# Optimization experiments

Measured on AMD Instinct MI355X. Metric: run time of the kernel, lower is better.

## Reference

```python
import jax, jax.numpy as jnp
import numpy as np

L, CIN, CKV, E, H, D, NQ, NK = 3, 128, 256, 128, 8, 16, 4096, 1024
CLAMP_MAX = 65503.0  # torch.clamp(max=65503)
SCALE = 1.0 / (D * D)  # non-standard: 1 / projection_dim**2


def group_norm(x, w, b, groups, eps=1e-5):
    # x: [..., C, N]; w, b broadcastable to x.shape[:-1] (i.e. lead + (C,))
    lead = x.shape[:-2]
    C, N = x.shape[-2:]
    xg = x.reshape(lead + (groups, C // groups, N))
    mu = xg.mean(axis=(-2, -1), keepdims=True)
    var = ((xg - mu) ** 2).mean(axis=(-2, -1), keepdims=True)
    xn = ((xg - mu) * jax.lax.rsqrt(var + eps)).reshape(lead + (C, N))
    return xn * w[..., None] + b[..., None]


def split_heads(t):
    # [L, 1, E, N] -> [L, 1, H, N, D]
    l, b, e, n = t.shape
    return t.transpose(0, 1, 3, 2).reshape(l, b, n, H, D).transpose(0, 1, 3, 2, 4)


def setup_inputs():
    key = jax.random.key(0)
    ks = jax.random.split(key, 18)
    r = lambda k, s: jax.random.normal(k, s, dtype=jnp.float32)
    return {
        'x': r(ks[0], (1, CIN, NQ)),
        'x_global': r(ks[1], (L, CKV, NK)),
        'xyz': r(ks[2], (1, NQ, 3)),
        'xyz_global': r(ks[3], (L, NK, 3)),
        'gn1_w': r(ks[4], (CIN,)), 'gn1_b': r(ks[5], (CIN,)),
        'gn2_w': r(ks[6], (L, CKV)), 'gn2_b': r(ks[7], (L, CKV)),
        'qw': r(ks[8], (L, E, CIN)) * 0.05, 'qb': r(ks[9], (L, E)),
        'kw': r(ks[10], (L, E, CKV)) * 0.05, 'kb': r(ks[11], (L, E)),
        'vw': r(ks[12], (L, E, CKV)) * 0.05, 'vb': r(ks[13], (L, E)),
        'qgn_w': r(ks[14], (L, E)), 'qgn_b': r(ks[15], (L, E)),
        'cw': r(ks[16], (L, CIN, E)) * 0.05, 'cb': r(ks[17], (L, CIN)),
    }


def reference(x, x_global, xyz, xyz_global, gn1_w, gn1_b, gn2_w, gn2_b,
              qw, qb, kw, kb, vw, vb, qgn_w, qgn_b, cw, cb):
    # pre-norm of query features (shared across layers): [1, CIN, NQ]
    xq = jax.nn.relu(group_norm(x, gn1_w, gn1_b, 8))
    # per-source KV features: [L, 1, CKV, NK]
    xg = jax.nn.relu(group_norm(x_global[:, None], gn2_w[:, None], gn2_b[:, None], 16))

    # conv1d (kernel=1) projections + the shared q_gn GroupNorm(8, E)
    q = jnp.einsum('lec,bcn->lben', qw, xq) + qb[:, None, :, None]        # [L,1,E,NQ]
    q = group_norm(q, qgn_w[:, None], qgn_b[:, None], 8)
    k = jnp.einsum('lec,lbcn->lben', kw, xg) + kb[:, None, :, None]       # [L,1,E,NK]
    k = group_norm(k, qgn_w[:, None], qgn_b[:, None], 8)
    v = jnp.einsum('lec,lbcn->lben', vw, xg) + vb[:, None, :, None]       # [L,1,E,NK]
    v = group_norm(v, qgn_w[:, None], qgn_b[:, None], 8)

    qh, kh, vh = split_heads(q), split_heads(k), split_heads(v)           # [L,1,H,*,D]

    score = jnp.einsum('lbhqd,lbhkd->lbhqk', qh * SCALE, kh)              # [L,1,H,NQ,NK]
    score = jnp.minimum(score, CLAMP_MAX)
    w_att = jax.nn.softmax(score, axis=-1)
    o = jnp.einsum('lbhqk,lbhkd->lbhqd', w_att, vh)                        # [L,1,H,NQ,D]
    o = o.transpose(0, 1, 3, 2, 4).reshape(L, 1, NQ, E)                    # merge heads
    o = jnp.einsum('lbqe,loe->lbqo', o, cw) + cb[:, None, None, :]         # combine heads
    o = o.transpose(0, 1, 3, 2) + xq[None]                                 # [L,1,CIN,NQ], SA residual

    out = o.mean(axis=0) + x                                               # mean over sources + block residual
    return out, w_att[-1]                                                  # weight of last layer, as in torch loop
```

## Files before the change

### kernel.cpp

```cpp
#include <hip/hip_runtime.h>
#include <math.h>

constexpr int NQ = 4096, NK = 1024, CIN = 128, CKV = 256, E = 128, H = 8, D = 16, LAYERS = 3;
constexpr float SCALE = 1.0f / 256.0f;
constexpr float CLAMP_MAX = 65503.0f;
constexpr float LOG2E = 1.44269504088896340736f;
constexpr float CLAMP2 = CLAMP_MAX * LOG2E;

typedef __bf16 bf16x8 __attribute__((ext_vector_type(8)));
typedef __bf16 bf16x4 __attribute__((ext_vector_type(4)));
typedef float f32x16 __attribute__((ext_vector_type(16)));
typedef float f32x4 __attribute__((ext_vector_type(4)));

__device__ __forceinline__ float exp2_fast(float x) {
#if __has_builtin(__builtin_amdgcn_exp2f)
  return __builtin_amdgcn_exp2f(x);
#else
  return exp2f(x);
#endif
}

__device__ __forceinline__ void block_reduce2(float& a, float& b, float* red) {
#pragma unroll
  for (int off = 32; off > 0; off >>= 1) {
    a += __shfl_down(a, off, 64);
    b += __shfl_down(b, off, 64);
  }
  int lane = threadIdx.x & 63, wid = threadIdx.x >> 6;
  if (lane == 0) { red[wid * 2] = a; red[wid * 2 + 1] = b; }
  __syncthreads();
  if (threadIdx.x == 0) {
    float sa = 0.f, sb = 0.f;
#pragma unroll
    for (int w = 0; w < 4; w++) { sa += red[w * 2]; sb += red[w * 2 + 1]; }
    red[0] = sa; red[1] = sb;
  }
  __syncthreads();
  a = red[0]; b = red[1];
}

__global__ __launch_bounds__(256) void pre_partial(const float* __restrict__ x,
                                                   const float* __restrict__ xg,
                                                   float* __restrict__ acc) {
  __shared__ float red[8];
  int b = blockIdx.x, t = threadIdx.x;
  const float4* p;
  int aidx;
  if (b < 256) { p = (const float4*)x + (size_t)b * 512; aidx = b >> 5; }
  else { int i = b - 256; p = (const float4*)xg + (size_t)i * 512; aidx = 8 + (i >> 3); }
  float s = 0.f, sq = 0.f;
#pragma unroll
  for (int i = 0; i < 2; i++) {
    float4 v = p[t + i * 256];
    s += v.x + v.y + v.z + v.w;
    sq += v.x * v.x + v.y * v.y + v.z * v.z + v.w * v.w;
  }
  block_reduce2(s, sq, red);
  if (t == 0) {
    atomicAdd(&acc[aidx * 2], s);
    atomicAdd(&acc[aidx * 2 + 1], sq);
  }
}

__global__ __launch_bounds__(256) void stage_a(const float* __restrict__ x,
                                               const float* __restrict__ xg,
                                               const float* __restrict__ acc,
                                               const float* __restrict__ gn1w,
                                               const float* __restrict__ gn1b,
                                               const float* __restrict__ gn2w,
                                               const float* __restrict__ gn2b,
                                               const float* __restrict__ qw,
                                               const float* __restrict__ kw,
                                               const float* __restrict__ vw,
                                               __bf16* __restrict__ xq_t,
                                               __bf16* __restrict__ xg_t,
                                               __bf16* __restrict__ qwb,
                                               __bf16* __restrict__ kwb,
                                               __bf16* __restrict__ vwb) {
  int b = blockIdx.x, t = threadIdx.x;
  if (b >= 320) {
    int i = b - 320;
    const float* src; __bf16* dst; int off;
    if (i < 24)      { src = qw; dst = qwb; off = i * 2048; }
    else if (i < 72) { src = kw; dst = kwb; off = (i - 24) * 2048; }
    else             { src = vw; dst = vwb; off = (i - 72) * 2048; }
    int base = off + t * 8;
    float4 a = *(const float4*)(src + base);
    float4 c = *(const float4*)(src + base + 4);
    bf16x8 o = { (__bf16)a.x, (__bf16)a.y, (__bf16)a.z, (__bf16)a.w,
                 (__bf16)c.x, (__bf16)c.y, (__bf16)c.z, (__bf16)c.w };
    *(bf16x8*)(dst + base) = o;
    return;
  }
  __shared__ float T[128 * 36];
  const float* in; __bf16* out; int N, Cout, ccbase, n0, gbase;
  const float* gw; const float* gb; float inv;
  if (b < 128) {
    in = x; N = NQ; out = xq_t; Cout = 128; ccbase = 0; n0 = b * 32;
    gw = gn1w; gb = gn1b; gbase = 0; inv = 1.f / 65536.f;
  } else {
    int i = b - 128; int l = i / 64; int r = i % 64; int ch = r >> 5;
    n0 = (r & 31) * 32;
    in = xg + ((size_t)l * 256 + ch * 128) * 1024; N = NK;
    out = xg_t + (size_t)l * 1024 * 256; Cout = 256; ccbase = ch * 128;
    gw = gn2w + l * 256 + ch * 128; gb = gn2b + l * 256 + ch * 128;
    gbase = 8 + l * 16 + ch * 8; inv = 1.f / 16384.f;
  }
  int nq = t & 7, cbase = t >> 3;
#pragma unroll
  for (int i = 0; i < 4; i++) {
    int c = cbase + 32 * i;
    int g = gbase + (c >> 4);
    float mu = acc[2 * g] * inv;
    float rs = rsqrtf(acc[2 * g + 1] * inv - mu * mu + 1e-5f);
    float sc = gw[c] * rs, sh = gb[c] - mu * sc;
    float4 v = *(const float4*)(in + (size_t)c * N + n0 + nq * 4);
    float4 o;
    o.x = fmaxf(v.x * sc + sh, 0.f);
    o.y = fmaxf(v.y * sc + sh, 0.f);
    o.z = fmaxf(v.z * sc + sh, 0.f);
    o.w = fmaxf(v.w * sc + sh, 0.f);
    *(float4*)(T + c * 36 + nq * 4) = o;
  }
  __syncthreads();
  int n = t >> 3, c0 = (t & 7) * 16;
  bf16x8 o1, o2;
#pragma unroll
  for (int j = 0; j < 8; j++) {
    o1[j] = (__bf16)T[(c0 + j) * 36 + n];
    o2[j] = (__bf16)T[(c0 + 8 + j) * 36 + n];
  }
  __bf16* op = out + (size_t)(n0 + n) * Cout + ccbase + c0;
  *(bf16x8*)op = o1;
  *(bf16x8*)(op + 8) = o2;
}

template <int KSTEPS>
__device__ __forceinline__ void gemm_tile(const __bf16* __restrict__ A,
                                          const __bf16* __restrict__ Bm,
                                          int stride, f32x16& acc, int l31, int half) {
#pragma unroll
  for (int ks = 0; ks < KSTEPS; ks++) {
    bf16x8 af = *(const bf16x8*)(A + (size_t)l31 * stride + ks * 16 + half * 8);
    bf16x8 bf = *(const bf16x8*)(Bm + (size_t)l31 * stride + ks * 16 + half * 8);
    acc = __builtin_amdgcn_mfma_f32_32x32x16_bf16(af, bf, acc, 0, 0, 0);
  }
}

__global__ __launch_bounds__(256) void proj_mfma(const __bf16* __restrict__ xq_t,
                                                 const __bf16* __restrict__ xg_t,
                                                 const __bf16* __restrict__ qwb,
                                                 const __bf16* __restrict__ kwb,
                                                 const __bf16* __restrict__ vwb,
                                                 const float* __restrict__ qb,
                                                 const float* __restrict__ kb,
                                                 const float* __restrict__ vb,
                                                 __bf16* __restrict__ q_raw,
                                                 __bf16* __restrict__ k_raw,
                                                 __bf16* __restrict__ v_raw,
                                                 float* __restrict__ qgnAcc) {
  int t = threadIdx.x;
  int w = blockIdx.x * 4 + (t >> 6);
  int lane = t & 63, l31 = lane & 31, half = lane >> 5;
  f32x16 acc = {0.f,0.f,0.f,0.f,0.f,0.f,0.f,0.f,0.f,0.f,0.f,0.f,0.f,0.f,0.f,0.f};
  int mat, l, e0, n0, N;
  const __bf16* A; const __bf16* Bm; const float* bias;
  if (w < 1536) {
    mat = 0; l = w >> 9; int r = w & 511; e0 = (r & 3) * 32; n0 = (r >> 2) * 32;
    N = NQ; A = qwb + (size_t)l * 128 * 128; Bm = xq_t; bias = qb + l * 128;
  } else if (w < 1920) {
    mat = 1; int idx = w - 1536; l = idx >> 7; int r = idx & 127;
    e0 = (r & 3) * 32; n0 = (r >> 2) * 32;
    N = NK; A = kwb + (size_t)l * 128 * 256; Bm = xg_t + (size_t)l * 1024 * 256;
    bias = kb + l * 128;
  } else {
    mat = 2; int idx = w - 1920; l = idx >> 7; int r = idx & 127;
    e0 = (r & 3) * 32; n0 = (r >> 2) * 32;
    N = NK; A = vwb + (size_t)l * 128 * 256; Bm = xg_t + (size_t)l * 1024 * 256;
    bias = vb + l * 128;
  }
  if (mat == 0) {
    gemm_tile<8>(A + (size_t)e0 * 128, Bm + (size_t)n0 * 128, 128, acc, l31, half);
  } else {
    gemm_tile<16>(A + (size_t)e0 * 256, Bm + (size_t)n0 * 256, 256, acc, l31, half);
  }

  float vals[16];
  float s0 = 0.f, sq0 = 0.f, s1 = 0.f, sq1 = 0.f;
#pragma unroll
  for (int r = 0; r < 16; r++) {
    int row = (r & 3) + 8 * (r >> 2) + 4 * half;
    float v = acc[r] + bias[e0 + row];
    vals[r] = v;
    if (r < 8) { s0 += v; sq0 += v * v; } else { s1 += v; sq1 += v * v; }
  }
#pragma unroll
  for (int off = 1; off < 64; off <<= 1) {
    s0 += __shfl_xor(s0, off); sq0 += __shfl_xor(sq0, off);
    s1 += __shfl_xor(s1, off); sq1 += __shfl_xor(sq1, off);
  }
  int gbase = (mat == 0 ? 0 : (mat == 1 ? 24 : 48)) + l * 8 + (e0 >> 4);
  if (lane == 0) {
    atomicAdd(&qgnAcc[gbase * 2], s0);
    atomicAdd(&qgnAcc[gbase * 2 + 1], sq0);
    atomicAdd(&qgnAcc[(gbase + 1) * 2], s1);
    atomicAdd(&qgnAcc[(gbase + 1) * 2 + 1], sq1);
  }
  if (mat < 2) {
    __bf16* out = (mat == 0 ? q_raw : k_raw);
#pragma unroll
    for (int qd = 0; qd < 4; qd++) {
      int h = (e0 >> 4) + (qd >> 1);
      int d0 = 4 * half + 8 * (qd & 1);
      bf16x4 o;
#pragma unroll
      for (int j = 0; j < 4; j++) o[j] = (__bf16)vals[qd * 4 + j];
      *(bf16x4*)(out + ((size_t)(l * 8 + h) * N + n0 + l31) * 16 + d0) = o;
    }
  } else {
#pragma unroll
    for (int r = 0; r < 16; r++) {
      int row = (r & 3) + 8 * (r >> 2) + 4 * half;
      int h = (e0 >> 4) + (row >> 4);
      v_raw[((size_t)(l * 8 + h) * 16 + (row & 15)) * NK + n0 + l31] = (__bf16)vals[r];
    }
  }
}

__global__ __launch_bounds__(256) void attn_kernel(const __bf16* __restrict__ qbf,
                                                   const __bf16* __restrict__ kbf,
                                                   const __bf16* __restrict__ vbf,
                                                   const float* __restrict__ qgnAcc,
                                                   const float* __restrict__ qgnw,
                                                   const float* __restrict__ qgnb,
                                                   float* __restrict__ ob,
                                                   float* __restrict__ rinv_ws) {
  __shared__ __bf16 Pt[4][32 * 40];
  __shared__ float rinv_s[4][32];

  const int t = threadIdx.x;
  const int wv = t >> 6;
  const int lane = t & 63;
  const int l31 = lane & 31, half = lane >> 5, l15 = lane & 15, quad = lane >> 4;
  const int h = blockIdx.y, l = blockIdx.z;
  const int q0 = blockIdx.x * 128 + wv * 32;

  const __bf16* Qh = qbf + (size_t)(l * H + h) * NQ * D;
  const __bf16* Kh = kbf + (size_t)(l * H + h) * NK * D;
  const __bf16* Vh = vbf + (size_t)(l * H + h) * D * NK;

  const int gq = l * 8 + h, gk = 24 + l * 8 + h, gv = 48 + l * 8 + h;
  const float invq = 1.f / 65536.f, invkv = 1.f / 16384.f;
  const float muq = qgnAcc[2 * gq] * invq;
  const float rsq = rsqrtf(qgnAcc[2 * gq + 1] * invq - muq * muq + 1e-5f);
  const float muk = qgnAcc[2 * gk] * invkv;
  const float rsk = rsqrtf(qgnAcc[2 * gk + 1] * invkv - muk * muk + 1e-5f);
  const float muv = qgnAcc[2 * gv] * invkv;
  const float rsv = rsqrtf(qgnAcc[2 * gv + 1] * invkv - muv * muv + 1e-5f);

  const int cbase = l * 128 + h * 16;
  float ka[8], kc[8];
  bf16x8 qfrag;
  {
    const float EX = SCALE * LOG2E;
    bf16x8 qraw = *(const bf16x8*)(Qh + (size_t)(q0 + l31) * D + half * 8);
#pragma unroll
    for (int j = 0; j < 8; j++) {
      float w = qgnw[cbase + half * 8 + j], bb = qgnb[cbase + half * 8 + j];
      float wq = w * rsq;
      qfrag[j] = (__bf16)((float)qraw[j] * (wq * EX) + (bb - muq * wq) * EX);
      float wk = w * rsk;
      ka[j] = wk; kc[j] = bb - muk * wk;
    }
  }
  const float va = qgnw[cbase + l15] * rsv;
  const float vc = qgnb[cbase + l15] - muv * va;

  f32x4 oa0 = {0.f, 0.f, 0.f, 0.f}, oa1 = {0.f, 0.f, 0.f, 0.f};
  float rsum[16];
#pragma unroll
  for (int r = 0; r < 16; ++r) rsum[r] = 0.f;

  __bf16* Pw = &Pt[wv][0];

  for (int c = 0; c < 32; ++c) {
    const int k0 = c * 32;
    bf16x8 kraw = *(const bf16x8*)(Kh + (size_t)(k0 + l31) * D + half * 8);
    bf16x8 kf;
#pragma unroll
    for (int j = 0; j < 8; j++) kf[j] = (__bf16)((float)kraw[j] * ka[j] + kc[j]);
    f32x16 s = {0.f,0.f,0.f,0.f,0.f,0.f,0.f,0.f,0.f,0.f,0.f,0.f,0.f,0.f,0.f,0.f};
    s = __builtin_amdgcn_mfma_f32_32x32x16_bf16(qfrag, kf, s, 0, 0, 0);
#pragma unroll
    for (int r = 0; r < 16; ++r) {
      float p = exp2_fast(fminf(s[r], CLAMP2));
      rsum[r] += p;
      int row = (r & 3) + 8 * (r >> 2) + 4 * half;
      Pw[row * 40 + l31] = (__bf16)p;
    }
    bf16x8 vraw = *(const bf16x8*)(Vh + (size_t)l15 * NK + k0 + quad * 8);
    bf16x8 bv;
#pragma unroll
    for (int j = 0; j < 8; j++) bv[j] = (__bf16)((float)vraw[j] * va + vc);
    bf16x8 a0 = *(const bf16x8*)(Pw + l15 * 40 + quad * 8);
    bf16x8 a1 = *(const bf16x8*)(Pw + (16 + l15) * 40 + quad * 8);
    oa0 = __builtin_amdgcn_mfma_f32_16x16x32_bf16(a0, bv, oa0, 0, 0, 0);
    oa1 = __builtin_amdgcn_mfma_f32_16x16x32_bf16(a1, bv, oa1, 0, 0, 0);
  }

#pragma unroll
  for (int r = 0; r < 16; ++r) {
    float v = rsum[r];
    v += __shfl_xor(v, 1); v += __shfl_xor(v, 2); v += __shfl_xor(v, 4);
    v += __shfl_xor(v, 8); v += __shfl_xor(v, 16);
    rsum[r] = v;
  }
  if (l31 == 0) {
#pragma unroll
    for (int r = 0; r < 16; ++r)
      rinv_s[wv][(r & 3) + 8 * (r >> 2) + 4 * half] = 1.f / rsum[r];
  }

  float* Ow = (float*)Pw;
#pragma unroll
  for (int r = 0; r < 4; ++r) {
    int qa = quad * 4 + r;
    Ow[l15 * 36 + qa] = oa0[r] * rinv_s[wv][qa];
    Ow[l15 * 36 + 16 + qa] = oa1[r] * rinv_s[wv][16 + qa];
  }
  if (l == 2 && lane < 32)
    rinv_ws[(size_t)h * NQ + q0 + lane] = rinv_s[wv][lane];
  {
    int dd = lane >> 2, j = (lane & 3) * 8;
    float4 u0 = *(const float4*)(Ow + dd * 36 + j);
    float4 u1 = *(const float4*)(Ow + dd * 36 + j + 4);
    size_t rb = (size_t)(l * E + h * D + dd) * NQ + q0 + j;
    *(float4*)(ob + rb) = u0;
    *(float4*)(ob + rb + 4) = u1;
  }
}

__global__ __launch_bounds__(256) void post_kernel(const __bf16* __restrict__ qbf,
                                                   const __bf16* __restrict__ kbf,
                                                   const float* __restrict__ rinv_ws,
                                                   const float* __restrict__ qgnAcc,
                                                   const float* __restrict__ qgnw,
                                                   const float* __restrict__ qgnb,
                                                   const float* __restrict__ x,
                                                   const float* __restrict__ accAll,
                                                   const float* __restrict__ gn1w,
                                                   const float* __restrict__ gn1b,
                                                   const float* __restrict__ ob,
                                                   const float* __restrict__ cw,
                                                   const float* __restrict__ cb,
                                                   float* __restrict__ out,
                                                   float* __restrict__ wout) {
  __shared__ float S[128 * 16];
  const int blk = blockIdx.x, t = threadIdx.x;
  if (blk < 512) {
    const int wv = t >> 6, lane = t & 63;
    const int l31 = lane & 31, half = lane >> 5;
    const int qtile = blk & 31, h = (blk >> 5) & 7, khalf = blk >> 8;
    const int q0 = qtile * 128 + wv * 32;
    const int kbase = khalf * 512;

    const __bf16* Qh = qbf + (size_t)(2 * H + h) * NQ * D;
    const __bf16* Kh = kbf + (size_t)(2 * H + h) * NK * D;

    const int gq = 16 + h, gk = 24 + 16 + h;
    const float invq = 1.f / 65536.f, invkv = 1.f / 16384.f;
    const float muq = qgnAcc[2 * gq] * invq;
    const float rsq = rsqrtf(qgnAcc[2 * gq + 1] * invq - muq * muq + 1e-5f);
    const float muk = qgnAcc[2 * gk] * invkv;
    const float rsk = rsqrtf(qgnAcc[2 * gk + 1] * invkv - muk * muk + 1e-5f);

    const int cbase = 2 * 128 + h * 16;
    float ka[8], kc[8];
    bf16x8 qfrag;
    {
      const float EX = SCALE * LOG2E;
      bf16x8 qraw = *(const bf16x8*)(Qh + (size_t)(q0 + l31) * D + half * 8);
#pragma unroll
      for (int j = 0; j < 8; j++) {
        float w = qgnw[cbase + half * 8 + j], bb = qgnb[cbase + half * 8 + j];
        float wq = w * rsq;
        qfrag[j] = (__bf16)((float)qraw[j] * (wq * EX) + (bb - muq * wq) * EX);
        float wk = w * rsk;
        ka[j] = wk; kc[j] = bb - muk * wk;
      }
    }

    float riv[16];
#pragma unroll
    for (int r = 0; r < 16; ++r)
      riv[r] = rinv_ws[(size_t)h * NQ + q0 + (r & 3) + 8 * (r >> 2) + 4 * half];

    for (int c = 0; c < 16; ++c) {
      const int k0 = kbase + c * 32;
      bf16x8 kraw = *(const bf16x8*)(Kh + (size_t)(k0 + l31) * D + half * 8);
      bf16x8 kf;
#pragma unroll
      for (int j = 0; j < 8; j++) kf[j] = (__bf16)((float)kraw[j] * ka[j] + kc[j]);
      f32x16 s = {0.f,0.f,0.f,0.f,0.f,0.f,0.f,0.f,0.f,0.f,0.f,0.f,0.f,0.f,0.f,0.f};
      s = __builtin_amdgcn_mfma_f32_32x32x16_bf16(qfrag, kf, s, 0, 0, 0);
#pragma unroll
      for (int r = 0; r < 16; ++r) {
        float p = exp2_fast(fminf(s[r], CLAMP2)) * riv[r];
        int row = (r & 3) + 8 * (r >> 2) + 4 * half;
        __builtin_nontemporal_store(p, &wout[(size_t)(h * NQ + q0 + row) * NK + k0 + l31]);
      }
    }
    return;
  }

  const int nt0 = (blk - 512) * 16;
  const int c0 = (t >> 2) * 2;
  const int nf = t & 3;
  float4 a0 = make_float4(0.f, 0.f, 0.f, 0.f);
  float4 a1 = make_float4(0.f, 0.f, 0.f, 0.f);
  for (int l = 0; l < LAYERS; l++) {
    if (l) __syncthreads();
#pragma unroll
    for (int i = 0; i < 2; i++) {
      int fid = i * 256 + t;
      int e = fid >> 2, pos = fid & 3;
      *(float4*)(S + e * 16 + pos * 4) =
          *(const float4*)(ob + ((size_t)l * E + e) * NQ + nt0 + pos * 4);
    }
    __syncthreads();
    const float* cwl = cw + (size_t)l * CIN * E;
#pragma unroll 8
    for (int e4 = 0; e4 < E / 4; e4++) {
      const int e = e4 * 4;
      float4 w0 = *(const float4*)(cwl + (size_t)c0 * E + e);
      float4 w1 = *(const float4*)(cwl + (size_t)(c0 + 1) * E + e);
      float4 s0 = *(const float4*)(S + (e + 0) * 16 + nf * 4);
      float4 s1 = *(const float4*)(S + (e + 1) * 16 + nf * 4);
      float4 s2 = *(const float4*)(S + (e + 2) * 16 + nf * 4);
      float4 s3 = *(const float4*)(S + (e + 3) * 16 + nf * 4);
      a0.x += w0.x * s0.x + w0.y * s1.x + w0.z * s2.x + w0.w * s3.x;
      a0.y += w0.x * s0.y + w0.y * s1.y + w0.z * s2.y + w0.w * s3.y;
      a0.z += w0.x * s0.z + w0.y * s1.z + w0.z * s2.z + w0.w * s3.z;
      a0.w += w0.x * s0.w + w0.y * s1.w + w0.z * s2.w + w0.w * s3.w;
      a1.x += w1.x * s0.x + w1.y * s1.x + w1.z * s2.x + w1.w * s3.x;
      a1.y += w1.x * s0.y + w1.y * s1.y + w1.z * s2.y + w1.w * s3.y;
      a1.z += w1.x * s0.z + w1.y * s1.z + w1.z * s2.z + w1.w * s3.z;
      a1.w += w1.x * s0.w + w1.y * s1.w + w1.z * s2.w + w1.w * s3.w;
    }
  }
  const float third = 1.f / 3.f;
#pragma unroll
  for (int i = 0; i < 2; i++) {
    int c = c0 + i;
    float4 a = i ? a1 : a0;
    float bsum = (cb[c] + cb[CIN + c] + cb[2 * CIN + c]) * third;
    int g = c >> 4;
    const float inv = 1.f / 65536.f;
    float mu = accAll[2 * g] * inv;
    float rs = rsqrtf(accAll[2 * g + 1] * inv - mu * mu + 1e-5f);
    float sc = gn1w[c] * rs, sh = gn1b[c] - mu * sc;
    size_t off = (size_t)c * NQ + nt0 + nf * 4;
    float4 xv = *(const float4*)(x + off);
    float4 o;
    o.x = xv.x + fmaxf(xv.x * sc + sh, 0.f) + a.x * third + bsum;
    o.y = xv.y + fmaxf(xv.y * sc + sh, 0.f) + a.y * third + bsum;
    o.z = xv.z + fmaxf(xv.z * sc + sh, 0.f) + a.z * third + bsum;
    o.w = xv.w + fmaxf(xv.w * sc + sh, 0.f) + a.w * third + bsum;
    *(float4*)(out + off) = o;
  }
}

extern "C" void kernel_launch(void* const* d_in, const int* in_sizes, int n_in,
                              void* d_out, int out_size, void* d_ws, size_t ws_size,
                              hipStream_t stream) {
  (void)in_sizes; (void)n_in; (void)out_size;
  const float* x    = (const float*)d_in[0];
  const float* xgi  = (const float*)d_in[1];
  const float* gn1w = (const float*)d_in[4];
  const float* gn1b = (const float*)d_in[5];
  const float* gn2w = (const float*)d_in[6];
  const float* gn2b = (const float*)d_in[7];
  const float* qw   = (const float*)d_in[8];
  const float* qb   = (const float*)d_in[9];
  const float* kw   = (const float*)d_in[10];
  const float* kb   = (const float*)d_in[11];
  const float* vw   = (const float*)d_in[12];
  const float* vb   = (const float*)d_in[13];
  const float* qgnw = (const float*)d_in[14];
  const float* qgnb = (const float*)d_in[15];
  const float* cw   = (const float*)d_in[16];
  const float* cb   = (const float*)d_in[17];

  float* ws = (float*)d_ws;
  __bf16* xq_t  = (__bf16*)ws;
  __bf16* xg_t  = (__bf16*)(ws + 262144);
  __bf16* qwb   = (__bf16*)(ws + 655360);
  __bf16* kwb   = (__bf16*)(ws + 679936);
  __bf16* vwb   = (__bf16*)(ws + 729088);
  __bf16* q_raw = (__bf16*)(ws + 778240);
  __bf16* k_raw = (__bf16*)(ws + 1564672);
  __bf16* v_raw = (__bf16*)(ws + 1761280);
  float*  ob    = ws + 1957888;
  float*  accAll = ws + 3530752;
  float*  rinv_ws = ws + 3531008;
  if (ws_size < (size_t)3563776 * sizeof(float)) return;

  float* qgnAcc = accAll + 112;
  float* outp = (float*)d_out;
  float* wout = outp + 524288;

  hipMemsetAsync(accAll, 0, 256 * sizeof(float), stream);

  pre_partial<<<640, 256, 0, stream>>>(x, xgi, accAll);

  stage_a<<<440, 256, 0, stream>>>(x, xgi, accAll, gn1w, gn1b, gn2w, gn2b,
                                   qw, kw, vw, xq_t, xg_t, qwb, kwb, vwb);

  proj_mfma<<<576, 256, 0, stream>>>(xq_t, xg_t, qwb, kwb, vwb, qb, kb, vb,
                                     q_raw, k_raw, v_raw, qgnAcc);

  attn_kernel<<<dim3(32, 8, 3), 256, 0, stream>>>(q_raw, k_raw, v_raw,
                                                  qgnAcc, qgnw, qgnb, ob, rinv_ws);

  post_kernel<<<768, 256, 0, stream>>>(q_raw, k_raw, rinv_ws, qgnAcc, qgnw, qgnb,
                                       x, accAll, gn1w, gn1b, ob, cw, cb, outp, wout);
}
```

Measured before the change: 289.3 us.

## Fold K/V group-norm affine into Q fragment and output; drop clamp; move weight cast

Rewrites the attention inner loop so the per-channel K group-norm scale is folded into the Q fragment and the K bias becomes a per-row additive term. The V affine is applied once to the normalized output, since softmax weights sum to one. Raw bf16 K and V now go straight into the MFMAs with no per-element conversion. The score clamp is removed, and the bf16 weight casting moves from stage_a into pre_partial. This cuts VALU work in the hot loop, but folding the K scale into bf16 Q can change rounding, and dropping the clamp assumes scores never exceed the limit.

```diff
diff --git a/kernel.cpp b/kernel.cpp
--- a/kernel.cpp
+++ b/kernel.cpp
@@ -3,9 +3,7 @@
 
 constexpr int NQ = 4096, NK = 1024, CIN = 128, CKV = 256, E = 128, H = 8, D = 16, LAYERS = 3;
 constexpr float SCALE = 1.0f / 256.0f;
-constexpr float CLAMP_MAX = 65503.0f;
 constexpr float LOG2E = 1.44269504088896340736f;
-constexpr float CLAMP2 = CLAMP_MAX * LOG2E;
 
 typedef __bf16 bf16x8 __attribute__((ext_vector_type(8)));
 typedef __bf16 bf16x4 __attribute__((ext_vector_type(4)));
@@ -41,45 +39,16 @@
 
 __global__ __launch_bounds__(256) void pre_partial(const float* __restrict__ x,
                                                    const float* __restrict__ xg,
-                                                   float* __restrict__ acc) {
-  __shared__ float red[8];
+                                                   const float* __restrict__ qw,
+                                                   const float* __restrict__ kw,
+                                                   const float* __restrict__ vw,
+                                                   float* __restrict__ acc,
+                                                   __bf16* __restrict__ qwb,
+                                                   __bf16* __restrict__ kwb,
+                                                   __bf16* __restrict__ vwb) {
   int b = blockIdx.x, t = threadIdx.x;
-  const float4* p;
-  int aidx;
-  if (b < 256) { p = (const float4*)x + (size_t)b * 512; aidx = b >> 5; }
-  else { int i = b - 256; p = (const float4*)xg + (size_t)i * 512; aidx = 8 + (i >> 3); }
-  float s = 0.f, sq = 0.f;
-#pragma unroll
-  for (int i = 0; i < 2; i++) {
-    float4 v = p[t + i * 256];
-    s += v.x + v.y + v.z + v.w;
-    sq += v.x * v.x + v.y * v.y + v.z * v.z + v.w * v.w;
-  }
-  block_reduce2(s, sq, red);
-  if (t == 0) {
-    atomicAdd(&acc[aidx * 2], s);
-    atomicAdd(&acc[aidx * 2 + 1], sq);
-  }
-}
-
-__global__ __launch_bounds__(256) void stage_a(const float* __restrict__ x,
-                                               const float* __restrict__ xg,
-                                               const float* __restrict__ acc,
-                                               const float* __restrict__ gn1w,
-                                               const float* __restrict__ gn1b,
-                                               const float* __restrict__ gn2w,
-                                               const float* __restrict__ gn2b,
-                                               const float* __restrict__ qw,
-                                               const float* __restrict__ kw,
-                                               const float* __restrict__ vw,
-                                               __bf16* __restrict__ xq_t,
-                                               __bf16* __restrict__ xg_t,
-                                               __bf16* __restrict__ qwb,
-                                               __bf16* __restrict__ kwb,
-                                               __bf16* __restrict__ vwb) {
-  int b = blockIdx.x, t = threadIdx.x;
-  if (b >= 320) {
-    int i = b - 320;
+  if (b >= 640) {
+    int i = b - 640;
     const float* src; __bf16* dst; int off;
     if (i < 24)      { src = qw; dst = qwb; off = i * 2048; }
     else if (i < 72) { src = kw; dst = kwb; off = (i - 24) * 2048; }
@@ -92,6 +61,35 @@
     *(bf16x8*)(dst + base) = o;
     return;
   }
+  __shared__ float red[8];
+  const float4* p;
+  int aidx;
+  if (b < 256) { p = (const float4*)x + (size_t)b * 512; aidx = b >> 5; }
+  else { int i = b - 256; p = (const float4*)xg + (size_t)i * 512; aidx = 8 + (i >> 3); }
+  float s = 0.f, sq = 0.f;
+#pragma unroll
+  for (int i = 0; i < 2; i++) {
+    float4 v = p[t + i * 256];
+    s += v.x + v.y + v.z + v.w;
+    sq += v.x * v.x + v.y * v.y + v.z * v.z + v.w * v.w;
+  }
+  block_reduce2(s, sq, red);
+  if (t == 0) {
+    atomicAdd(&acc[aidx * 2], s);
+    atomicAdd(&acc[aidx * 2 + 1], sq);
+  }
+}
+
+__global__ __launch_bounds__(256) void stage_a(const float* __restrict__ x,
+                                               const float* __restrict__ xg,
+                                               const float* __restrict__ acc,
+                                               const float* __restrict__ gn1w,
+                                               const float* __restrict__ gn1b,
+                                               const float* __restrict__ gn2w,
+                                               const float* __restrict__ gn2b,
+                                               __bf16* __restrict__ xq_t,
+                                               __bf16* __restrict__ xg_t) {
+  int b = blockIdx.x, t = threadIdx.x;
   __shared__ float T[128 * 36];
   const float* in; __bf16* out; int N, Cout, ccbase, n0, gbase;
   const float* gw; const float* gb; float inv;
@@ -259,8 +257,8 @@
   const float rsv = rsqrtf(qgnAcc[2 * gv + 1] * invkv - muv * muv + 1e-5f);
 
   const int cbase = l * 128 + h * 16;
-  float ka[8], kc[8];
   bf16x8 qfrag;
+  float bq_part = 0.f;
   {
     const float EX = SCALE * LOG2E;
     bf16x8 qraw = *(const bf16x8*)(Qh + (size_t)(q0 + l31) * D + half * 8);
@@ -268,11 +266,19 @@
     for (int j = 0; j < 8; j++) {
       float w = qgnw[cbase + half * 8 + j], bb = qgnb[cbase + half * 8 + j];
       float wq = w * rsq;
-      qfrag[j] = (__bf16)((float)qraw[j] * (wq * EX) + (bb - muq * wq) * EX);
+      float qe = (float)qraw[j] * (wq * EX) + (bb - muq * wq) * EX;
       float wk = w * rsk;
-      ka[j] = wk; kc[j] = bb - muk * wk;
-    }
-  }
+      float ck = bb - muk * wk;
+      qfrag[j] = (__bf16)(qe * wk);
+      bq_part += qe * ck;
+    }
+  }
+  const float bq = bq_part + __shfl_xor(bq_part, 32);
+  float bqr[16];
+#pragma unroll
+  for (int r = 0; r < 16; ++r)
+    bqr[r] = __shfl(bq, (r & 3) + 8 * (r >> 2) + 4 * half);
+
   const float va = qgnw[cbase + l15] * rsv;
   const float vc = qgnb[cbase + l15] - muv * va;
 
@@ -285,25 +291,19 @@
 
   for (int c = 0; c < 32; ++c) {
     const int k0 = c * 32;
-    bf16x8 kraw = *(const bf16x8*)(Kh + (size_t)(k0 + l31) * D + half * 8);
-    bf16x8 kf;
-#pragma unroll
-    for (int j = 0; j < 8; j++) kf[j] = (__bf16)((float)kraw[j] * ka[j] + kc[j]);
+    bf16x8 kf = *(const bf16x8*)(Kh + (size_t)(k0 + l31) * D + half * 8);
     f32x16 s = {0.f,0.f,0.f,0.f,0.f,0.f,0.f,0.f,0.f,0.f,0.f,0.f,0.f,0.f,0.f,0.f};
     s = __builtin_amdgcn_mfma_f32_32x32x16_bf16(qfrag, kf, s, 0, 0, 0);
 #pragma unroll
     for (int r = 0; r < 16; ++r) {
-      float p = exp2_fast(fminf(s[r], CLAMP2));
+      float p = exp2_fast(s[r] + bqr[r]);
       rsum[r] += p;
       int row = (r & 3) + 8 * (r >> 2) + 4 * half;
       Pw[row * 40 + l31] = (__bf16)p;
     }
-    bf16x8 vraw = *(const bf16x8*)(Vh + (size_t)l15 * NK + k0 + quad * 8);
-    bf16x8 bv;
-#pragma unroll
-    for (int j = 0; j < 8; j++) bv[j] = (__bf16)((float)vraw[j] * va + vc);
     bf16x8 a0 = *(const bf16x8*)(Pw + l15 * 40 + quad * 8);
     bf16x8 a1 = *(const bf16x8*)(Pw + (16 + l15) * 40 + quad * 8);
+    bf16x8 bv = *(const bf16x8*)(Vh + (size_t)l15 * NK + k0 + quad * 8);
     oa0 = __builtin_amdgcn_mfma_f32_16x16x32_bf16(a0, bv, oa0, 0, 0, 0);
     oa1 = __builtin_amdgcn_mfma_f32_16x16x32_bf16(a1, bv, oa1, 0, 0, 0);
   }
@@ -325,8 +325,8 @@
 #pragma unroll
   for (int r = 0; r < 4; ++r) {
     int qa = quad * 4 + r;
-    Ow[l15 * 36 + qa] = oa0[r] * rinv_s[wv][qa];
-    Ow[l15 * 36 + 16 + qa] = oa1[r] * rinv_s[wv][16 + qa];
+    Ow[l15 * 36 + qa] = oa0[r] * rinv_s[wv][qa] * va + vc;
+    Ow[l15 * 36 + 16 + qa] = oa1[r] * rinv_s[wv][16 + qa] * va + vc;
   }
   if (l == 2 && lane < 32)
     rinv_ws[(size_t)h * NQ + q0 + lane] = rinv_s[wv][lane];
@@ -375,8 +375,8 @@
     const float rsk = rsqrtf(qgnAcc[2 * gk + 1] * invkv - muk * muk + 1e-5f);
 
     const int cbase = 2 * 128 + h * 16;
-    float ka[8], kc[8];
     bf16x8 qfrag;
+    float bq_part = 0.f;
     {
       const float EX = SCALE * LOG2E;
       bf16x8 qraw = *(const bf16x8*)(Qh + (size_t)(q0 + l31) * D + half * 8);
@@ -384,11 +384,18 @@
       for (int j = 0; j < 8; j++) {
         float w = qgnw[cbase + half * 8 + j], bb = qgnb[cbase + half * 8 + j];
         float wq = w * rsq;
-        qfrag[j] = (__bf16)((float)qraw[j] * (wq * EX) + (bb - muq * wq) * EX);
+        float qe = (float)qraw[j] * (wq * EX) + (bb - muq * wq) * EX;
         float wk = w * rsk;
-        ka[j] = wk; kc[j] = bb - muk * wk;
+        float ck = bb - muk * wk;
+        qfrag[j] = (__bf16)(qe * wk);
+        bq_part += qe * ck;
       }
     }
+    const float bq = bq_part + __shfl_xor(bq_part, 32);
+    float bqr[16];
+#pragma unroll
+    for (int r = 0; r < 16; ++r)
+      bqr[r] = __shfl(bq, (r & 3) + 8 * (r >> 2) + 4 * half);
 
     float riv[16];
 #pragma unroll
@@ -397,15 +404,12 @@
 
     for (int c = 0; c < 16; ++c) {
       const int k0 = kbase + c * 32;
-      bf16x8 kraw = *(const bf16x8*)(Kh + (size_t)(k0 + l31) * D + half * 8);
-      bf16x8 kf;
-#pragma unroll
-      for (int j = 0; j < 8; j++) kf[j] = (__bf16)((float)kraw[j] * ka[j] + kc[j]);
+      bf16x8 kf = *(const bf16x8*)(Kh + (size_t)(k0 + l31) * D + half * 8);
       f32x16 s = {0.f,0.f,0.f,0.f,0.f,0.f,0.f,0.f,0.f,0.f,0.f,0.f,0.f,0.f,0.f,0.f};
       s = __builtin_amdgcn_mfma_f32_32x32x16_bf16(qfrag, kf, s, 0, 0, 0);
 #pragma unroll
       for (int r = 0; r < 16; ++r) {
-        float p = exp2_fast(fminf(s[r], CLAMP2)) * riv[r];
+        float p = exp2_fast(s[r] + bqr[r]) * riv[r];
         int row = (r & 3) + 8 * (r >> 2) + 4 * half;
         __builtin_nontemporal_store(p, &wout[(size_t)(h * NQ + q0 + row) * NK + k0 + l31]);
       }
@@ -511,10 +515,9 @@
 
   hipMemsetAsync(accAll, 0, 256 * sizeof(float), stream);
 
-  pre_partial<<<640, 256, 0, stream>>>(x, xgi, accAll);
-
-  stage_a<<<440, 256, 0, stream>>>(x, xgi, accAll, gn1w, gn1b, gn2w, gn2b,
-                                   qw, kw, vw, xq_t, xg_t, qwb, kwb, vwb);
+  pre_partial<<<760, 256, 0, stream>>>(x, xgi, qw, kw, vw, accAll, qwb, kwb, vwb);
+
+  stage_a<<<320, 256, 0, stream>>>(x, xgi, accAll, gn1w, gn1b, gn2w, gn2b, xq_t, xg_t);
 
   proj_mfma<<<576, 256, 0, stream>>>(xq_t, xg_t, qwb, kwb, vwb, qb, kb, vb,
                                      q_raw, k_raw, v_raw, qgnAcc);
```

After: 281.1 us. -2.8%, faster.
